# Kernel optimization log

Hardware: AMD Instinct MI355X
Metric: run time of the kernel (lower is better)

The kernel has to match this reference:

```python
import jax, jax.numpy as jnp
import numpy as np

KS = 3
PAD = 1


def _deform_conv3d(x, offset, weight, ks=KS, padding=PAD):
    N = offset.shape[1] // 3          # = ks**3
    b, c = x.shape[0], x.shape[1]
    h, w, d = offset.shape[2], offset.shape[3], offset.shape[4]
    if padding:
        x = jnp.pad(x, ((0, 0), (0, 0), (padding, padding), (padding, padding), (padding, padding)))
    H, W, D = x.shape[2], x.shape[3], x.shape[4]
    dt = offset.dtype

    # kernel-relative offsets p_n  [3N]
    r = jnp.arange(-(ks - 1) // 2, (ks - 1) // 2 + 1)
    kx, ky, kz = jnp.meshgrid(r, r, r, indexing='ij')
    p_n = jnp.concatenate([kx.ravel(), ky.ravel(), kz.ravel()]).astype(dt)
    # base grid p_0 (1..h etc., in padded coords)  [3N,h,w,d]
    gx, gy, gz = jnp.meshgrid(jnp.arange(1, h + 1), jnp.arange(1, w + 1), jnp.arange(1, d + 1), indexing='ij')
    p_0 = jnp.concatenate([jnp.broadcast_to(g[None], (N, h, w, d)) for g in (gx, gy, gz)], axis=0).astype(dt)

    p = p_0[None] + p_n[None, :, None, None, None] + offset   # [b,3N,h,w,d]
    p = jnp.transpose(p, (0, 2, 3, 4, 1))                     # [b,h,w,d,3N]

    def split3(t):
        return t[..., :N], t[..., N:2 * N], t[..., 2 * N:]

    q_lt = jnp.floor(jax.lax.stop_gradient(p))
    q_rb = q_lt + 1
    ltx, lty, ltz = split3(q_lt)
    rbx, rby, rbz = split3(q_rb)
    q0x = jnp.clip(ltx, 0, H - 1).astype(jnp.int32)
    q0y = jnp.clip(lty, 0, W - 1).astype(jnp.int32)
    q0z = jnp.clip(ltz, 0, D - 1).astype(jnp.int32)
    q1x = jnp.clip(rbx, 0, H - 1).astype(jnp.int32)
    q1y = jnp.clip(rby, 0, W - 1).astype(jnp.int32)
    q1z = jnp.clip(rbz, 0, D - 1).astype(jnp.int32)

    px, py, pz = split3(p)
    # out-of-range mask (detached); snap those points to floor, then clamp
    mx = jax.lax.stop_gradient(((px < padding) | (px > H - 1 - padding)).astype(dt))
    my = jax.lax.stop_gradient(((py < padding) | (py > W - 1 - padding)).astype(dt))
    mz = jax.lax.stop_gradient(((pz < padding) | (pz > D - 1 - padding)).astype(dt))
    px = jnp.clip(px * (1 - mx) + jnp.floor(px) * mx, 0, H - 1)
    py = jnp.clip(py * (1 - my) + jnp.floor(py) * my, 0, W - 1)
    pz = jnp.clip(pz * (1 - mz) + jnp.floor(pz) * mz, 0, D - 1)

    # trilinear weights per axis
    lx = 1 + (q0x.astype(dt) - px); hx = 1 - (q1x.astype(dt) - px)
    ly = 1 + (q0y.astype(dt) - py); hy = 1 - (q1y.astype(dt) - py)
    lz = 1 + (q0z.astype(dt) - pz); hz = 1 - (q1z.astype(dt) - pz)

    x_flat = x.reshape(b, c, H * W * D)

    def gather(qx, qy, qz):
        idx = (qx * (W * D) + qy * D + qz).reshape(b, -1)     # [b, h*w*d*N]
        out = jax.vmap(lambda xf, i: xf[:, i])(x_flat, idx)   # [b, c, h*w*d*N]
        return out.reshape(b, c, h, w, d, N)

    corners = [
        (q0x, q0y, q0z, lx * ly * lz), (q1x, q1y, q1z, hx * hy * hz),
        (q0x, q0y, q1z, lx * ly * hz), (q0x, q1y, q0z, lx * hy * lz),
        (q0x, q1y, q1z, lx * hy * hz), (q1x, q0y, q0z, hx * ly * lz),
        (q1x, q0y, q1z, hx * ly * hz), (q1x, q1y, q0z, hx * hy * lz),
    ]
    xo = jnp.zeros((b, c, h, w, d, N), dtype=dt)
    for qx, qy, qz, g in corners:
        xo = xo + g[:, None] * gather(qx, qy, qz)

    # rearrange into consecutive ks^3 blocks: [b,c,h*ks,w*ks,d*ks]
    xo = jnp.concatenate([xo[..., s:s + ks * ks].reshape(b, c, h, w, d * ks * ks)
                          for s in range(0, N, ks * ks)], axis=-1)
    M = xo.shape[4]
    xo = jnp.concatenate([xo[..., s:s + d * ks * ks].reshape(b, c, h, w * ks, d * ks)
                          for s in range(0, M, d * ks * ks)], axis=-1)
    xo = xo.reshape(b, c, h * ks, w * ks, d * ks)

    # grouped-stride conv: kernel ks, stride ks, no bias
    return jax.lax.conv_general_dilated(
        xo, weight, window_strides=(ks, ks, ks), padding='VALID',
        dimension_numbers=('NCDHW', 'OIDHW', 'NCDHW'))


def setup_inputs() -> dict:
    key = jax.random.key(0)
    k1, k2, k3 = jax.random.split(key, 3)
    B, C, S = 1, 16, 32
    x = jax.random.normal(k1, (B, C, S, S, S), dtype=jnp.float32)
    offset = jax.random.normal(k2, (B, 81, S, S, S), dtype=jnp.float32)
    weight = jax.random.normal(k3, (16, C, 3, 3, 3), dtype=jnp.float32) * 0.05
    return {"x": x, "offset": offset, "weight": weight}


def reference(x, offset, weight):
    return _deform_conv3d(x, offset, weight)
```

## Files before the change

### kernel.cpp

```cpp
#include <hip/hip_runtime.h>


#define NCH 16
#define PADDIM 34
#define PLANE 32768

typedef float f4 __attribute__((ext_vector_type(4)));
typedef _Float16 h4 __attribute__((ext_vector_type(4)));
typedef short bh8 __attribute__((ext_vector_type(8)));
typedef float fx16 __attribute__((ext_vector_type(16)));

__device__ __forceinline__ f4 f4fma(float s, const f4 a, const f4 b) {
  f4 r;
  r.x = fmaf(s, a.x, b.x); r.y = fmaf(s, a.y, b.y);
  r.z = fmaf(s, a.z, b.z); r.w = fmaf(s, a.w, b.w);
  return r;
}

__device__ __forceinline__ short bfbits(float f) {
  unsigned u = __float_as_uint(f);
  u += 0x7FFFu + ((u >> 16) & 1u);
  return (short)(u >> 16);
}

__device__ __forceinline__ void axis_interp(float p, int& q0, int& q1,
                                            float& lo, float& hi) {
  float fl = floorf(p);
  int fi = (int)fl;
  q0 = min(max(fi, 0), 33);
  q1 = min(max(fi + 1, 0), 33);
  float pm = (p < 1.f || p > 32.f) ? fl : p;
  pm = fminf(fmaxf(pm, 0.f), 33.f);
  lo = 1.f + (float)q0 - pm;
  hi = 1.f - (float)q1 + pm;
}

__global__ void prep_small(const float* __restrict__ x,
                           const float* __restrict__ W,
                           unsigned char* __restrict__ xq,
                           unsigned short* __restrict__ wtb) {
  int b = blockIdx.x;
  if (b < 2457) {
    int idx = b * 256 + threadIdx.x;
    if (idx >= PADDIM * PADDIM * PADDIM * NCH) return;
    int c = idx & 15;
    int site = idx >> 4;
    int qz = site % PADDIM;
    int t = site / PADDIM;
    int qy = t % PADDIM;
    int qx = t / PADDIM;
    float v = 0.f;
    if (qx >= 1 && qx <= 32 && qy >= 1 && qy <= 32 && qz >= 1 && qz <= 32)
      v = x[c * PLANE + ((qx - 1) * 32 + (qy - 1)) * 32 + (qz - 1)];
    v = fminf(fmaxf(v, -5.f), 5.f) * 25.4f;
    xq[idx] = (unsigned char)((int)rintf(v) + 128);
  } else {
    int idx = (b - 2457) * 256 + threadIdx.x;
    if (idx >= 6912) return;
    int j = idx & 7;
    int o = (idx >> 3) & 15;
    int h = (idx >> 7) & 1;
    int t = idx >> 8;
    int cin = 8 * h + j;
    float val = W[(o * 16 + cin) * 27 + t] * (5.f / 127.f);
    unsigned u = __float_as_uint(val);
    u += 0x7FFFu + ((u >> 16) & 1u);
    wtb[idx] = (unsigned short)(u >> 16);
  }
}

__global__ __launch_bounds__(512, 4) void deform_main16(
    const float* __restrict__ off, const unsigned short* __restrict__ Wtb,
    const unsigned char* __restrict__ xq, float* __restrict__ out) {
  __shared__ float sOff[2916];
  __shared__ bh8 sWtB[864];
  __shared__ uint4 sX[9 * 9 * 34];
  __shared__ _Float16 redH[8][16][36];

  int tid = threadIdx.x;
  int b = blockIdx.x;
  int xcd = b & 7;
  int local = b >> 3;
  int i = xcd * 4 + (local & 3);
  int j = local >> 2;

  int x0 = min(max(i - 3, 0), 25);
  int y0 = min(max(j - 3, 0), 25);

  const uint4* xq4 = (const uint4*)xq;

  {
    const f4* wtg = (const f4*)Wtb;
    f4* d = (f4*)sWtB;
    for (int s = tid; s < 864; s += 512) d[s] = wtg[s];
  }
  for (int s = tid; s < 9 * 9 * 34; s += 512) {
    int qz = s % 34;
    int rc = s / 34;
    int dy = rc % 9;
    int dx = rc / 9;
    sX[s] = xq4[((x0 + dx) * PADDIM + (y0 + dy)) * PADDIM + qz];
  }
#pragma unroll
  for (int it = 0; it < 6; it++) {
    int s = tid + it * 512;
    if (s < 2916) {
      int comp = s / 972;
      int rem = s - comp * 972;
      int alpha = rem / 324;
      int rem2 = rem - alpha * 324;
      int n = rem2 / 12;
      int pos = rem2 - n * 12;
      int aj = 2 * alpha + j;
      int r3 = aj % 3;
      int wp = 10 * alpha + aj / 3;
      int dp = min((r3 * 96) / 9 + pos, 31);
      sOff[s] = __builtin_nontemporal_load(
          &off[(comp * 27 + n) * PLANE + i * 1024 + wp * 32 + dp]);
    }
  }
  __syncthreads();

  int kk = tid & 31;
  int cslot = (tid >> 5) & 1;
  int th = tid >> 6;
  int om = tid & 15;

  fx16 acc = {0.f, 0.f, 0.f, 0.f, 0.f, 0.f, 0.f, 0.f,
              0.f, 0.f, 0.f, 0.f, 0.f, 0.f, 0.f, 0.f};

#pragma unroll
  for (int c = 0; c < 4; c++) {
    int t = th + 8 * c;
    if (t < 27) {
      int alpha = t / 9;
      int t3 = t / 3;
      int beta = t3 % 3;
      int gamma = t - t3 * 3;
      int G = 3072 * alpha + 96 * j + 3 * kk + gamma;
      int wp = G / 288;
      int u = G - wp * 288;
      int dp = u / 9;
      int m = u - dp * 9;
      int n = 9 * beta + m;
      int aj = 2 * alpha + j;
      int dp_lo = ((aj % 3) * 96) / 9;
      int lidx = (alpha * 27 + n) * 12 + (dp - dp_lo);

      float ox = sOff[lidx];
      float oy = sOff[lidx + 972];
      float oz = sOff[lidx + 1944];

      int md3 = m / 3;
      float px = (float)(i + beta) + ox;
      float py = (float)(wp + md3) + oy;
      float pz = (float)(dp + m - md3 * 3) + oz;

      int q0x, q1x, q0y, q1y, q0z, q1z;
      float lx, hx, ly, hy, lz, hz;
      axis_interp(px, q0x, q1x, lx, hx);
      axis_interp(py, q0y, q1y, ly, hy);
      axis_interp(pz, q0z, q1z, lz, hz);

      float wz = cslot ? hz : lz;
      int qzs = cslot ? q1z : q0z;
      float wsum = (lx + hx) * (ly + hy) * wz;

      bh8 bf = sWtB[(t * 2 + cslot) * 16 + om];

      float s[16];
#pragma unroll
      for (int cc = 0; cc < 16; cc++) s[cc] = 0.f;

#pragma unroll
      for (int g = 0; g < 4; g++) {
        int qx = (g & 2) ? q1x : q0x;
        int qy = (g & 1) ? q1y : q0y;
        float w = ((g & 2) ? hx : lx) * ((g & 1) ? hy : ly) * wz;
        int dx = qx - x0;
        int dy = qy - y0;
        bool in = ((unsigned)dx < 9u) && ((unsigned)dy < 9u);
        int laddr = in ? (dx * 9 + dy) * 34 + qzs : 0;
        uint4 v = sX[laddr];
        if (!in)
          v = xq4[(qx * PADDIM + qy) * PADDIM + qzs];
        unsigned wd[4] = {v.x, v.y, v.z, v.w};
#pragma unroll
        for (int nn = 0; nn < 4; nn++) {
          unsigned wv = wd[nn];
          s[4 * nn + 0] = fmaf(w, (float)(wv & 0xff), s[4 * nn + 0]);
          s[4 * nn + 1] = fmaf(w, (float)((wv >> 8) & 0xff), s[4 * nn + 1]);
          s[4 * nn + 2] = fmaf(w, (float)((wv >> 16) & 0xff), s[4 * nn + 2]);
          s[4 * nn + 3] = fmaf(w, (float)(wv >> 24), s[4 * nn + 3]);
        }
      }

      float wsum_t = wsum + __shfl_xor(wsum, 32);
      bh8 af;
#pragma unroll
      for (int jj = 0; jj < 8; jj++) {
        float send = cslot ? s[jj] : s[jj + 8];
        float recv = __shfl_xor(send, 32);
        float own = cslot ? s[jj + 8] : s[jj];
        float a = fmaf(-128.f, wsum_t, own + recv);
        af[jj] = bfbits(a);
      }

      acc = __builtin_amdgcn_mfma_f32_32x32x16_bf16(af, bf, acc, 0, 0, 0);
    }
  }

  if (((tid >> 4) & 1) == 0) {
    _Float16* base = &redH[th][om][0];
#pragma unroll
    for (int r4 = 0; r4 < 4; r4++) {
      h4 v;
      v.x = (_Float16)acc[4 * r4 + 0];
      v.y = (_Float16)acc[4 * r4 + 1];
      v.z = (_Float16)acc[4 * r4 + 2];
      v.w = (_Float16)acc[4 * r4 + 3];
      *(h4*)&base[8 * r4 + 4 * cslot] = v;
    }
  }
  __syncthreads();

  int o = tid >> 5;
  int kr = tid & 31;
  float v = 0.f;
#pragma unroll
  for (int g = 0; g < 8; g++) v += (float)redH[g][o][kr];
  __builtin_nontemporal_store(v, &out[((o * 32 + i) * 32 + j) * 32 + kr]);
}

__device__ __forceinline__ void tap_meta(int t, int i, int j, int k,
                                         int& src, float& bx, float& by,
                                         float& bz) {
  int alpha = t / 9;
  int beta = (t / 3) % 3;
  int gamma = t - (t / 3) * 3;
  int G = 3072 * alpha + 96 * j + 3 * k + gamma;
  int wp = G / 288;
  int u = G - wp * 288;
  int dp = u / 9;
  int m = u - dp * 9;
  int n = 9 * beta + m;
  src = n * PLANE + i * 1024 + wp * 32 + dp;
  int md3 = m / 3;
  bx = (float)(i + beta);
  by = (float)(wp + md3);
  bz = (float)(dp + m - md3 * 3);
}

__device__ __forceinline__ f4 corner_direct(const float* __restrict__ x,
                                            int qx, int qy, int qz, int c0) {
  f4 r = {0.f, 0.f, 0.f, 0.f};
  if (qx < 1 || qx > 32 || qy < 1 || qy > 32 || qz < 1 || qz > 32) return r;
  int bi = ((qx - 1) * 32 + (qy - 1)) * 32 + (qz - 1);
  const float* xb = x + c0 * PLANE + bi;
  r.x = xb[0]; r.y = xb[PLANE]; r.z = xb[2 * PLANE]; r.w = xb[3 * PLANE];
  return r;
}

__global__ __launch_bounds__(256) void deform_fallback(
    const float* __restrict__ x, const float* __restrict__ offset,
    const float* __restrict__ W, float* __restrict__ out) {
  __shared__ float red[8][32][20];

  int tid = threadIdx.x;
  int k = tid & 31;
  int c4 = (tid >> 5) & 3;
  int th = tid >> 7;
  int i = blockIdx.x >> 5;
  int j = blockIdx.x & 31;

  f4 acc0 = {0.f, 0.f, 0.f, 0.f};
  f4 acc1 = acc0, acc2 = acc0, acc3 = acc0;

  for (int t = th; t < 27; t += 2) {
    int src;
    float bx, by, bz;
    tap_meta(t, i, j, k, src, bx, by, bz);
    float px = bx + offset[src];
    float py = by + offset[src + 27 * PLANE];
    float pz = bz + offset[src + 54 * PLANE];

    int q0x, q1x, q0y, q1y, q0z, q1z;
    float lx, hx, ly, hy, lz, hz;
    axis_interp(px, q0x, q1x, lx, hx);
    axis_interp(py, q0y, q1y, ly, hy);
    axis_interp(pz, q0z, q1z, lz, hz);

    float a00 = ly * lz, a01 = ly * hz, a10 = hy * lz, a11 = hy * hz;
    float w000 = lx * a00, w001 = lx * a01, w010 = lx * a10, w011 = lx * a11;
    float w100 = hx * a00, w101 = hx * a01, w110 = hx * a10, w111 = hx * a11;

    int c0 = c4 * 4;
    f4 s4 = {0.f, 0.f, 0.f, 0.f};
    s4 = f4fma(w000, corner_direct(x, q0x, q0y, q0z, c0), s4);
    s4 = f4fma(w001, corner_direct(x, q0x, q0y, q1z, c0), s4);
    s4 = f4fma(w010, corner_direct(x, q0x, q1y, q0z, c0), s4);
    s4 = f4fma(w011, corner_direct(x, q0x, q1y, q1z, c0), s4);
    s4 = f4fma(w100, corner_direct(x, q1x, q0y, q0z, c0), s4);
    s4 = f4fma(w101, corner_direct(x, q1x, q0y, q1z, c0), s4);
    s4 = f4fma(w110, corner_direct(x, q1x, q1y, q0z, c0), s4);
    s4 = f4fma(w111, corner_direct(x, q1x, q1y, q1z, c0), s4);

    float sarr[4] = {s4.x, s4.y, s4.z, s4.w};
#pragma unroll
    for (int cc = 0; cc < 4; cc++) {
      float s = sarr[cc];
      const float* wr = W + (c4 * 4 + cc) * 27 + t;
      acc0.x = fmaf(s, wr[0 * 432], acc0.x);
      acc0.y = fmaf(s, wr[1 * 432], acc0.y);
      acc0.z = fmaf(s, wr[2 * 432], acc0.z);
      acc0.w = fmaf(s, wr[3 * 432], acc0.w);
      acc1.x = fmaf(s, wr[4 * 432], acc1.x);
      acc1.y = fmaf(s, wr[5 * 432], acc1.y);
      acc1.z = fmaf(s, wr[6 * 432], acc1.z);
      acc1.w = fmaf(s, wr[7 * 432], acc1.w);
      acc2.x = fmaf(s, wr[8 * 432], acc2.x);
      acc2.y = fmaf(s, wr[9 * 432], acc2.y);
      acc2.z = fmaf(s, wr[10 * 432], acc2.z);
      acc2.w = fmaf(s, wr[11 * 432], acc2.w);
      acc3.x = fmaf(s, wr[12 * 432], acc3.x);
      acc3.y = fmaf(s, wr[13 * 432], acc3.y);
      acc3.z = fmaf(s, wr[14 * 432], acc3.z);
      acc3.w = fmaf(s, wr[15 * 432], acc3.w);
    }
  }

  int grp = th * 4 + c4;
  float* r = &red[grp][k][0];
  ((f4*)r)[0] = acc0;
  ((f4*)r)[1] = acc1;
  ((f4*)r)[2] = acc2;
  ((f4*)r)[3] = acc3;
  __syncthreads();

#pragma unroll
  for (int rep = 0; rep < 2; rep++) {
    int idx = tid + rep * 256;
    int o = idx >> 5;
    int kk2 = idx & 31;
    float v = 0.f;
#pragma unroll
    for (int g = 0; g < 8; g++) v += red[g][kk2][o];
    out[((o * 32 + i) * 32 + j) * 32 + kk2] = v;
  }
}

extern "C" void kernel_launch(void* const* d_in, const int* in_sizes, int n_in,
                              void* d_out, int out_size, void* d_ws, size_t ws_size,
                              hipStream_t stream) {
  const float* x = (const float*)d_in[0];
  const float* off = (const float*)d_in[1];
  const float* W = (const float*)d_in[2];
  float* out = (float*)d_out;

  const size_t WTB_B = 6912 * 2;
  const size_t XQ_B = (size_t)PADDIM * PADDIM * PADDIM * NCH;
  const size_t NEED = WTB_B + XQ_B;

  if (ws_size >= NEED) {
    unsigned short* wtb = (unsigned short*)d_ws;
    unsigned char* xq = (unsigned char*)d_ws + WTB_B;
    prep_small<<<2457 + 27, 256, 0, stream>>>(x, W, xq, wtb);
    deform_main16<<<1024, 512, 0, stream>>>(off, wtb, xq, out);
  } else {
    deform_fallback<<<1024, 256, 0, stream>>>(x, off, W, out);
  }
}
```

Measured before the change: 91.08 us.

## Split work across lanes by channel half instead of z-corner, dropping shuffles

Each lane pair previously split the trilinear gather by z-corner: each lane loaded all 16 channels for 4 corners and then swapped halves through cross-lane shuffles. Now each lane gathers all 8 corners but loads only its 8-channel half (a uint2 instead of a uint4). This removes the 9 shuffles per tap and halves the accumulator registers, at the cost of twice as many gather loads per lane. The launch bound min-blocks hint is also relaxed from 4 to 2, which lets the compiler use more registers per thread.

```diff
diff --git a/kernel.cpp b/kernel.cpp
--- a/kernel.cpp
+++ b/kernel.cpp
@@ -69,7 +69,7 @@
   }
 }
 
-__global__ __launch_bounds__(512, 4) void deform_main16(
+__global__ __launch_bounds__(512, 2) void deform_main16(
     const float* __restrict__ off, const unsigned short* __restrict__ Wtb,
     const unsigned char* __restrict__ xq, float* __restrict__ out) {
   __shared__ float sOff[2916];
@@ -88,6 +88,7 @@
   int y0 = min(max(j - 3, 0), 25);
 
   const uint4* xq4 = (const uint4*)xq;
+  const uint2* xq2 = (const uint2*)xq;
 
   {
     const f4* wtg = (const f4*)Wtb;
@@ -126,6 +127,8 @@
   int th = tid >> 6;
   int om = tid & 15;
 
+  const uint2* sX2 = (const uint2*)sX;
+
   fx16 acc = {0.f, 0.f, 0.f, 0.f, 0.f, 0.f, 0.f, 0.f,
               0.f, 0.f, 0.f, 0.f, 0.f, 0.f, 0.f, 0.f};
 
@@ -162,47 +165,45 @@
       axis_interp(py, q0y, q1y, ly, hy);
       axis_interp(pz, q0z, q1z, lz, hz);
 
-      float wz = cslot ? hz : lz;
-      int qzs = cslot ? q1z : q0z;
-      float wsum = (lx + hx) * (ly + hy) * wz;
+      float wsum_t = (lx + hx) * (ly + hy) * (lz + hz);
 
       bh8 bf = sWtB[(t * 2 + cslot) * 16 + om];
 
-      float s[16];
-#pragma unroll
-      for (int cc = 0; cc < 16; cc++) s[cc] = 0.f;
-
-#pragma unroll
-      for (int g = 0; g < 4; g++) {
-        int qx = (g & 2) ? q1x : q0x;
-        int qy = (g & 1) ? q1y : q0y;
-        float w = ((g & 2) ? hx : lx) * ((g & 1) ? hy : ly) * wz;
+      float wxy[4] = {lx * ly, lx * hy, hx * ly, hx * hy};
+
+      float s[8];
+#pragma unroll
+      for (int cc = 0; cc < 8; cc++) s[cc] = 0.f;
+
+#pragma unroll
+      for (int g = 0; g < 8; g++) {
+        int qx = (g & 4) ? q1x : q0x;
+        int qy = (g & 2) ? q1y : q0y;
+        int qz = (g & 1) ? q1z : q0z;
+        float w = wxy[g >> 1] * ((g & 1) ? hz : lz);
         int dx = qx - x0;
         int dy = qy - y0;
         bool in = ((unsigned)dx < 9u) && ((unsigned)dy < 9u);
-        int laddr = in ? (dx * 9 + dy) * 34 + qzs : 0;
-        uint4 v = sX[laddr];
+        int s16 = (dx * 9 + dy) * 34 + qz;
+        uint2 v = sX2[(in ? s16 : 0) * 2 + cslot];
         if (!in)
-          v = xq4[(qx * PADDIM + qy) * PADDIM + qzs];
-        unsigned wd[4] = {v.x, v.y, v.z, v.w};
-#pragma unroll
-        for (int nn = 0; nn < 4; nn++) {
-          unsigned wv = wd[nn];
-          s[4 * nn + 0] = fmaf(w, (float)(wv & 0xff), s[4 * nn + 0]);
-          s[4 * nn + 1] = fmaf(w, (float)((wv >> 8) & 0xff), s[4 * nn + 1]);
-          s[4 * nn + 2] = fmaf(w, (float)((wv >> 16) & 0xff), s[4 * nn + 2]);
-          s[4 * nn + 3] = fmaf(w, (float)(wv >> 24), s[4 * nn + 3]);
-        }
+          v = xq2[((qx * PADDIM + qy) * PADDIM + qz) * 2 + cslot];
+        unsigned wv = v.x;
+        s[0] = fmaf(w, (float)(wv & 0xff), s[0]);
+        s[1] = fmaf(w, (float)((wv >> 8) & 0xff), s[1]);
+        s[2] = fmaf(w, (float)((wv >> 16) & 0xff), s[2]);
+        s[3] = fmaf(w, (float)(wv >> 24), s[3]);
+        wv = v.y;
+        s[4] = fmaf(w, (float)(wv & 0xff), s[4]);
+        s[5] = fmaf(w, (float)((wv >> 8) & 0xff), s[5]);
+        s[6] = fmaf(w, (float)((wv >> 16) & 0xff), s[6]);
+        s[7] = fmaf(w, (float)(wv >> 24), s[7]);
       }
 
-      float wsum_t = wsum + __shfl_xor(wsum, 32);
       bh8 af;
 #pragma unroll
       for (int jj = 0; jj < 8; jj++) {
-        float send = cslot ? s[jj] : s[jj + 8];
-        float recv = __shfl_xor(send, 32);
-        float own = cslot ? s[jj + 8] : s[jj];
-        float a = fmaf(-128.f, wsum_t, own + recv);
+        float a = fmaf(-128.f, wsum_t, s[jj]);
         af[jj] = bfbits(a);
       }
 
```

After: 94.89 us. +4.2%, slower.
